# Kernel optimization log

Hardware: AMD Instinct MI355X
Metric: run time of the kernel (lower is better)

## Reference

```python
import jax, jax.numpy as jnp
import numpy as np

N = 100000   # nodes
E = 1600000  # edges (before self loops)
F = 64       # num_features
H = 64       # hidden_channels
C = 10       # num_classes
G = 128      # graphs in batch
NEG_SLOPE = 0.2


def setup_inputs() -> dict:
    key = jax.random.key(0)
    ks = jax.random.split(key, 16)
    x = jax.random.normal(ks[0], (N, F), dtype=jnp.float32)
    edge_index = jax.random.randint(ks[1], (2, E), 0, N, dtype=jnp.int64)
    batch = jnp.sort(jax.random.randint(ks[2], (N,), 0, G, dtype=jnp.int64))
    def glorot(k, shape):
        fan = shape[0] + shape[-1]
        return jax.random.uniform(k, shape, jnp.float32, -1.0, 1.0) * np.sqrt(6.0 / fan)
    return {
        "x": x, "edge_index": edge_index, "batch": batch,
        # GATConv 1 (F -> H)
        "W1": glorot(ks[3], (F, H)), "as1": glorot(ks[4], (H,)), "ad1": glorot(ks[5], (H,)), "b1": jnp.zeros((H,), jnp.float32),
        # GATConv 2 (H -> H)
        "W2": glorot(ks[6], (H, H)), "as2": glorot(ks[7], (H,)), "ad2": glorot(ks[8], (H,)), "b2": jnp.zeros((H,), jnp.float32),
        # MLP head
        "mw1": glorot(ks[9], (H, H)), "mb1": jnp.zeros((H,), jnp.float32),
        "mw2": glorot(ks[10], (H, C)), "mb2": jnp.zeros((C,), jnp.float32),
    }


def gat_conv(x, src, dst, W, a_s, a_d, b):
    # x: [N, Fin] -> h: [N, Fout]
    h = x @ W
    # per-node attention halves, gathered per edge (heads=1)
    al_s = h @ a_s   # [N]
    al_d = h @ a_d   # [N]
    e = jax.nn.leaky_relu(al_s[src] + al_d[dst], NEG_SLOPE)  # [E']
    # segment softmax over incoming edges of each destination node
    m = jax.ops.segment_max(e, dst, num_segments=N)
    ex = jnp.exp(e - m[dst])
    denom = jax.ops.segment_sum(ex, dst, num_segments=N)
    alpha = ex / denom[dst]                                   # [E']
    # weighted scatter-add of source features
    out = jax.ops.segment_sum(alpha[:, None] * h[src], dst, num_segments=N)
    return out + b


def reference(x, edge_index, batch, W1, as1, ad1, b1, W2, as2, ad2, b2, mw1, mb1, mw2, mb2):
    # add self loops (PyG GATConv default)
    loop = jnp.arange(N, dtype=edge_index.dtype)
    src = jnp.concatenate([edge_index[0], loop])
    dst = jnp.concatenate([edge_index[1], loop])

    h = gat_conv(x, src, dst, W1, as1, ad1, b1)
    h = jax.nn.elu(h)  # dropout p=0.5 is identity in eval mode
    h = gat_conv(h, src, dst, W2, as2, ad2, b2)
    h = jax.nn.elu(h)

    h = jax.nn.relu(h @ mw1 + mb1) @ mw2 + mb2   # MLP [N, C]
    return jax.ops.segment_sum(h, batch, num_segments=G)  # global_add_pool [G, C]
```

## Files before the change

kernel.cpp:

```cpp
#include <hip/hip_runtime.h>
#include <hip/hip_bf16.h>
#include <math.h>

#define SHIFT 20.0f
#define T_PER 16
#define TILE (256 * T_PER)
#define SEG_CAP 12288
#define BCAP 10240

typedef __bf16 bf16x8 __attribute__((ext_vector_type(8)));
typedef float  f32x4  __attribute__((ext_vector_type(4)));

__device__ __forceinline__ unsigned f2bf(float f) {
    unsigned u = __float_as_uint(f);
    return (u + 0x7fffu + ((u >> 16) & 1u)) >> 16;
}

__global__ void init_kernel(int* __restrict__ bcur, int K2,
                            float* __restrict__ Pz, int nPz)
{
    int t = threadIdx.x;
    if (t < K2) bcur[t * 16] = t * BCAP;
    for (int i = t; i < nPz; i += 256) Pz[i] = 0.f;
}

__global__ __launch_bounds__(256) void multisplit_kernel(
    const int* __restrict__ esrc, const int* __restrict__ edst,
    int* __restrict__ bcur, unsigned* __restrict__ pairbuf,
    int nE, int nN, int K2, int nTiles)
{
    __shared__ int lhist[256];
    __shared__ int lbase[256];
    int t = threadIdx.x;
    int tot = nE + nN;

    for (int tile = blockIdx.x; tile < nTiles; tile += gridDim.x) {
        int base = tile * TILE;
        if (t < K2) lhist[t] = 0;
        __syncthreads();

        unsigned pk[T_PER];
        int loc[T_PER];
        #pragma unroll
        for (int i = 0; i < T_PER; i++) {
            int e = base + t + i * 256;
            if (e < tot) {
                int s = (e < nE) ? esrc[e] : (e - nE);
                int d = (e < nE) ? edst[e] : (e - nE);
                int b = d >> 9;
                pk[i] = ((unsigned)s << 9) | (unsigned)(d & 511);
                int idx = atomicAdd(&lhist[b], 1);
                loc[i] = (b << 20) | idx;
            } else loc[i] = -1;
        }
        __syncthreads();
        if (t < K2) {
            int c = lhist[t];
            lbase[t] = (c > 0) ? atomicAdd(&bcur[t * 16], c) : 0;
        }
        __syncthreads();
        #pragma unroll
        for (int i = 0; i < T_PER; i++) {
            if (loc[i] >= 0)
                pairbuf[lbase[loc[i] >> 20] + (loc[i] & 0xFFFFF)] = pk[i];
        }
        __syncthreads();
    }
}

__global__ __launch_bounds__(256) void local_scatter_kernel(
    const unsigned* __restrict__ pairbuf, const int* __restrict__ bcur,
    int2* __restrict__ rp2, int* __restrict__ csr_src, int nN, int K2)
{
    __shared__ unsigned seg[SEG_CAP];
    __shared__ int lh[512];
    __shared__ int cur[512];
    __shared__ int psum[256];
    int b = blockIdx.x;
    int t = threadIdx.x;
    int d0 = b * 512;
    int nd = min(512, nN - d0);
    int lo = b * BCAP;
    int hi = bcur[b * 16];
    int len = hi - lo;
    bool inLds = (len <= SEG_CAP);

    lh[t] = 0; lh[t + 256] = 0;
    if (inLds)
        for (int j = t; j < len; j += 256) seg[j] = pairbuf[lo + j];
    __syncthreads();
    if (inLds) {
        for (int j = t; j < len; j += 256) atomicAdd(&lh[seg[j] & 511u], 1);
    } else {
        for (int j = lo + t; j < hi; j += 256)
            atomicAdd(&lh[pairbuf[j] & 511u], 1);
    }
    __syncthreads();

    int v0 = lh[2 * t], v1 = lh[2 * t + 1];
    int ps = v0 + v1;
    psum[t] = ps;
    __syncthreads();
    for (int off = 1; off < 256; off <<= 1) {
        int u = (t >= off) ? psum[t - off] : 0;
        __syncthreads();
        psum[t] += u;
        __syncthreads();
    }
    int e0 = lo + psum[t] - ps;
    int e1 = e0 + v0;
    cur[2 * t] = e0;
    cur[2 * t + 1] = e1;
    if (2 * t < nd)     rp2[d0 + 2 * t]     = make_int2(e0, v0);
    if (2 * t + 1 < nd) rp2[d0 + 2 * t + 1] = make_int2(e1, v1);
    __syncthreads();

    if (inLds) {
        for (int j = t; j < len; j += 256) {
            unsigned w = seg[j];
            int pos = atomicAdd(&cur[w & 511u], 1);
            csr_src[pos] = (int)(w >> 9);
        }
    } else {
        for (int j = lo + t; j < hi; j += 256) {
            unsigned w = pairbuf[j];
            int pos = atomicAdd(&cur[w & 511u], 1);
            csr_src[pos] = (int)(w >> 9);
        }
    }
}

__global__ void prep_kernel(const float* __restrict__ W1,
                            const float* __restrict__ as1, const float* __restrict__ ad1,
                            const float* __restrict__ W2,
                            const float* __restrict__ as2, const float* __restrict__ ad2,
                            const float* __restrict__ mw1,
                            uint4* __restrict__ Wf1, uint4* __restrict__ Wf2,
                            uint4* __restrict__ mwf)
{
    __shared__ float wasad[256];
    int t = threadIdx.x;
    {
        int k = t & 63;
        const float* W  = (t < 128) ? W1 : W2;
        const float* av = (t < 64) ? as1 : (t < 128) ? ad1 : (t < 192) ? as2 : ad2;
        float s = 0.f;
        for (int n = 0; n < 64; n++) s = fmaf(W[k * 64 + n], av[n], s);
        wasad[t] = s;
    }
    __syncthreads();

    for (int idx = t; idx < 1792; idx += 256) {
        const float* W; const float* wv; uint4* dst; int rem;
        if (idx < 640)       { rem = idx;        W = W1;  wv = &wasad[0];   dst = Wf1; }
        else if (idx < 1280) { rem = idx - 640;  W = W2;  wv = &wasad[128]; dst = Wf2; }
        else                 { rem = idx - 1280; W = mw1; wv = nullptr;     dst = mwf; }
        int pair = rem >> 6, l = rem & 63;
        int tt = pair >> 1, s = pair & 1;
        int kb = s * 32 + (l >> 4) * 8;
        unsigned d[4];
        if (tt < 4) {
            int n = tt * 16 + (l & 15);
            #pragma unroll
            for (int j = 0; j < 4; j++)
                d[j] = f2bf(W[(kb + 2 * j) * 64 + n]) |
                       (f2bf(W[(kb + 2 * j + 1) * 64 + n]) << 16);
        } else {
            int n0 = l & 15;
            #pragma unroll
            for (int j = 0; j < 4; j++) {
                float v0 = (n0 == 0) ? wv[kb + 2 * j]     : (n0 == 1) ? wv[64 + kb + 2 * j]     : 0.f;
                float v1 = (n0 == 0) ? wv[kb + 2 * j + 1] : (n0 == 1) ? wv[64 + kb + 2 * j + 1] : 0.f;
                d[j] = f2bf(v0) | (f2bf(v1) << 16);
            }
        }
        dst[pair * 64 + l] = make_uint4(d[0], d[1], d[2], d[3]);
    }
}

__global__ __launch_bounds__(256) void gemm_att_mfma(
    const void* __restrict__ Xv, int x_is_bf16,
    const uint4* __restrict__ Wf,
    __hip_bfloat16* __restrict__ Hout,
    float* __restrict__ als, float* __restrict__ ald, int nN)
{
    __shared__ __align__(16) unsigned char lds[256 * 144];
    int t = threadIdx.x, lane = t & 63, wv = t >> 6;
    int b0 = blockIdx.x * 256;

    uint4 wf[10];
    #pragma unroll
    for (int p = 0; p < 10; p++) wf[p] = Wf[p * 64 + lane];

    if (x_is_bf16) {
        const uint4* X4 = (const uint4*)Xv;
        int limit = nN * 8;
        #pragma unroll
        for (int k = 0; k < 8; k++) {
            int dst = t + k * 256;
            int idx = b0 * 8 + dst;
            if (idx < limit) {
                int r = dst >> 3, c = dst & 7;
                *(uint4*)(lds + r * 144 + c * 16) = X4[idx];
            }
        }
    } else {
        const float4* Xf = (const float4*)Xv;
        int limit = nN * 16;
        #pragma unroll
        for (int k = 0; k < 16; k++) {
            int dst = t + k * 256;
            int idx = b0 * 16 + dst;
            if (idx < limit) {
                float4 v = Xf[idx];
                uint2 r2;
                r2.x = f2bf(v.x) | (f2bf(v.y) << 16);
                r2.y = f2bf(v.z) | (f2bf(v.w) << 16);
                int r = dst >> 4, c = dst & 15;
                *(uint2*)(lds + r * 144 + c * 8) = r2;
            }
        }
    }
    __syncthreads();

    f32x4 acc[4][5] = {};
    int rbase = wv * 64;
    #pragma unroll
    for (int s = 0; s < 2; s++) {
        #pragma unroll
        for (int rf = 0; rf < 4; rf++) {
            const uint4 av = *(const uint4*)(lds + (rbase + rf * 16 + (lane & 15)) * 144
                                                 + s * 64 + (lane >> 4) * 16);
            bf16x8 a = __builtin_bit_cast(bf16x8, av);
            #pragma unroll
            for (int tt = 0; tt < 5; tt++) {
                bf16x8 b = __builtin_bit_cast(bf16x8, wf[tt * 2 + s]);
                acc[rf][tt] = __builtin_amdgcn_mfma_f32_16x16x32_bf16(a, b, acc[rf][tt], 0, 0, 0);
            }
        }
    }

    int q = lane >> 4, c = lane & 15;
    #pragma unroll
    for (int rf = 0; rf < 4; rf++) {
        #pragma unroll
        for (int r = 0; r < 4; r++) {
            int n = b0 + rbase + rf * 16 + q * 4 + r;
            if (n < nN) {
                #pragma unroll
                for (int tt = 0; tt < 4; tt++)
                    Hout[(size_t)n * 64 + tt * 16 + c] = __float2bfloat16(acc[rf][tt][r]);
                if (c == 0)      als[n] = acc[rf][4][r];
                else if (c == 1) ald[n] = acc[rf][4][r];
            }
        }
    }
}

__global__ __launch_bounds__(256) void pull_kernel(
    const int* __restrict__ csr_src, const int2* __restrict__ rp2,
    const unsigned* __restrict__ Hu,
    const float* __restrict__ als, const float* __restrict__ ald,
    const float* __restrict__ bias,
    __hip_bfloat162* __restrict__ out2, int nN)
{
    int lane = threadIdx.x & 63;
    int half = lane >> 5;
    int fl = lane & 31;
    int wid  = (blockIdx.x * blockDim.x + threadIdx.x) >> 6;
    int nw   = (gridDim.x * blockDim.x) >> 6;
    float2 bl2 = ((const float2*)bias)[fl];

    for (int d = wid; d < nN; d += nw) {
        int2 rp = rp2[d];
        int s0 = rp.x, s1 = rp.x + rp.y;
        float aldd = ald[d];
        float aclo = 0.f, achi = 0.f, den = 0.f;

        for (int base = s0; base < s1; base += 64) {
            int j = base + lane;
            bool v = (j < s1);
            int sl = v ? csr_src[j] : 0;
            float ex = 0.f;
            if (v) {
                float sc = als[sl] + aldd;
                sc = (sc > 0.f) ? sc : 0.2f * sc;
                ex = __expf(sc - SHIFT);
            }
            float es = ex;
            #pragma unroll
            for (int off = 32; off > 0; off >>= 1) es += __shfl_xor(es, off);
            den += es;

            int m = min(64, s1 - base);
            int i2 = 0;
            for (; i2 + 3 < m; i2 += 4) {
                int iA = i2 + half, iB = i2 + 2 + half;
                int sA = __shfl(sl, iA), sB = __shfl(sl, iB);
                float eA = __shfl(ex, iA), eB = __shfl(ex, iB);
                unsigned dA = Hu[(size_t)sA * 32 + fl];
                unsigned dB = Hu[(size_t)sB * 32 + fl];
                aclo = fmaf(eA, __uint_as_float(dA << 16), aclo);
                achi = fmaf(eA, __uint_as_float(dA & 0xffff0000u), achi);
                aclo = fmaf(eB, __uint_as_float(dB << 16), aclo);
                achi = fmaf(eB, __uint_as_float(dB & 0xffff0000u), achi);
            }
            for (; i2 < m; i2 += 2) {
                int idx = i2 + half;
                int s = __shfl(sl, idx);
                float e = (idx < m) ? __shfl(ex, idx) : 0.f;
                unsigned dd = Hu[(size_t)s * 32 + fl];
                aclo = fmaf(e, __uint_as_float(dd << 16), aclo);
                achi = fmaf(e, __uint_as_float(dd & 0xffff0000u), achi);
            }
        }
        aclo += __shfl_xor(aclo, 32);
        achi += __shfl_xor(achi, 32);
        float v0 = aclo / den + bl2.x;
        float v1 = achi / den + bl2.y;
        v0 = (v0 > 0.f) ? v0 : expm1f(v0);
        v1 = (v1 > 0.f) ? v1 : expm1f(v1);
        if (half == 0) {
            __hip_bfloat162 pk;
            pk.x = __float2bfloat16(v0);
            pk.y = __float2bfloat16(v1);
            out2[(size_t)d * 32 + fl] = pk;
        }
    }
}

__global__ __launch_bounds__(256) void mlp_pool_mfma(
    const uint4* __restrict__ Hin,
    const uint4* __restrict__ mwf, const float* __restrict__ mb1,
    const int* __restrict__ batch,
    float* __restrict__ P, float* __restrict__ Pcnt, int nN)
{
    __shared__ __align__(16) unsigned char lds[256 * 144];
    int t = threadIdx.x, lane = t & 63, wv = t >> 6;
    int b0 = blockIdx.x * 256;

    uint4 wf[8];
    #pragma unroll
    for (int p = 0; p < 8; p++) wf[p] = mwf[p * 64 + lane];

    int limit = nN * 8;
    #pragma unroll
    for (int k = 0; k < 8; k++) {
        int dst = t + k * 256;
        int idx = b0 * 8 + dst;
        if (idx < limit) {
            int r = dst >> 3, c = dst & 7;
            *(uint4*)(lds + r * 144 + c * 16) = Hin[idx];
        }
    }
    __syncthreads();

    f32x4 acc[4][4] = {};
    int rbase = wv * 64;
    #pragma unroll
    for (int s = 0; s < 2; s++) {
        #pragma unroll
        for (int rf = 0; rf < 4; rf++) {
            const uint4 av = *(const uint4*)(lds + (rbase + rf * 16 + (lane & 15)) * 144
                                                 + s * 64 + (lane >> 4) * 16);
            bf16x8 a = __builtin_bit_cast(bf16x8, av);
            #pragma unroll
            for (int tt = 0; tt < 4; tt++) {
                bf16x8 b = __builtin_bit_cast(bf16x8, wf[tt * 2 + s]);
                acc[rf][tt] = __builtin_amdgcn_mfma_f32_16x16x32_bf16(a, b, acc[rf][tt], 0, 0, 0);
            }
        }
    }

    int q = lane >> 4, c = lane & 15;
    float bl0 = mb1[c], bl1 = mb1[16 + c], bl2 = mb1[32 + c], bl3 = mb1[48 + c];
    float r0 = 0.f, r1 = 0.f, r2 = 0.f, r3 = 0.f, ccnt = 0.f;
    int gcur = -1;
    #pragma unroll
    for (int rf = 0; rf < 4; rf++) {
        #pragma unroll
        for (int r = 0; r < 4; r++) {
            int n = b0 + rbase + rf * 16 + q * 4 + r;
            if (n < nN) {
                int g = batch[n];
                if (g != gcur) {
                    if (gcur >= 0) {
                        atomicAdd(&P[(size_t)gcur * 64 + c],      r0);
                        atomicAdd(&P[(size_t)gcur * 64 + 16 + c], r1);
                        atomicAdd(&P[(size_t)gcur * 64 + 32 + c], r2);
                        atomicAdd(&P[(size_t)gcur * 64 + 48 + c], r3);
                        if (c == 0) atomicAdd(&Pcnt[gcur], ccnt);
                    }
                    gcur = g; r0 = r1 = r2 = r3 = 0.f; ccnt = 0.f;
                }
                r0 += fmaxf(acc[rf][0][r] + bl0, 0.f);
                r1 += fmaxf(acc[rf][1][r] + bl1, 0.f);
                r2 += fmaxf(acc[rf][2][r] + bl2, 0.f);
                r3 += fmaxf(acc[rf][3][r] + bl3, 0.f);
                ccnt += 1.f;
            }
        }
    }
    if (gcur >= 0) {
        atomicAdd(&P[(size_t)gcur * 64 + c],      r0);
        atomicAdd(&P[(size_t)gcur * 64 + 16 + c], r1);
        atomicAdd(&P[(size_t)gcur * 64 + 32 + c], r2);
        atomicAdd(&P[(size_t)gcur * 64 + 48 + c], r3);
        if (c == 0) atomicAdd(&Pcnt[gcur], ccnt);
    }
}

__global__ void head_out_kernel(const float* __restrict__ P,
                                const float* __restrict__ Pcnt,
                                const float* __restrict__ mw2,
                                const float* __restrict__ mb2,
                                float* __restrict__ out, int nOut)
{
    int t = blockIdx.x * blockDim.x + threadIdx.x;
    if (t >= nOut) return;
    int g = t / 10, j = t % 10;
    float s = mb2[j] * Pcnt[g];
    const float* pr = P + (size_t)g * 64;
    #pragma unroll
    for (int k = 0; k < 64; k++) s = fmaf(pr[k], mw2[k * 10 + j], s);
    out[t] = s;
}

extern "C" void kernel_launch(void* const* d_in, const int* in_sizes, int n_in,
                              void* d_out, int out_size, void* d_ws, size_t ws_size,
                              hipStream_t stream)
{
    const float* x   = (const float*)d_in[0];
    const int*  eidx = (const int*)d_in[1];
    const int* batch = (const int*)d_in[2];
    const float* W1  = (const float*)d_in[3];
    const float* as1 = (const float*)d_in[4];
    const float* ad1 = (const float*)d_in[5];
    const float* b1  = (const float*)d_in[6];
    const float* W2  = (const float*)d_in[7];
    const float* as2 = (const float*)d_in[8];
    const float* ad2 = (const float*)d_in[9];
    const float* b2  = (const float*)d_in[10];
    const float* mw1 = (const float*)d_in[11];
    const float* mb1 = (const float*)d_in[12];
    const float* mw2 = (const float*)d_in[13];
    const float* mb2 = (const float*)d_in[14];
    float* out = (float*)d_out;

    int nN = in_sizes[0] / 64;
    int nE = in_sizes[1] / 2;
    int tot = nE + nN;
    int K2 = (nN + 511) >> 9;
    int G  = out_size / 10;
    const int* esrc = eidx;
    const int* edst = eidx + nE;

    float* ws = (float*)d_ws;
    size_t NF = (size_t)nN * 64;
    size_t capTot = (size_t)K2 * BCAP;
    float* bufA   = ws;
    float* bufB   = ws + NF;
    float* als    = ws + 2 * NF;
    float* ald    = als + nN;
    int2* rp2     = (int2*)(ald + nN);
    int* csr_src  = (int*)(rp2 + nN);
    int* bcur     = csr_src + capTot;
    float* P      = (float*)(bcur + K2 * 16 + 15);
    float* Pcnt   = P + (size_t)G * 64;
    uintptr_t wb  = ((uintptr_t)(Pcnt + G) + 255) & ~(uintptr_t)255;
    uint4* Wf1    = (uint4*)wb;
    uint4* Wf2    = Wf1 + 640;
    uint4* mwf    = Wf2 + 640;
    unsigned* pairbuf = (unsigned*)bufA;
    __hip_bfloat16* hbf = (__hip_bfloat16*)bufB;

    dim3 blk(256);
    int nTiles = (tot + TILE - 1) / TILE;
    int nT256 = (nN + 255) / 256;

    init_kernel<<<1, blk, 0, stream>>>(bcur, K2, P, G * 64 + G);
    multisplit_kernel<<<nTiles, blk, 0, stream>>>(esrc, edst, bcur, pairbuf,
                                                  nE, nN, K2, nTiles);
    local_scatter_kernel<<<K2, blk, 0, stream>>>(pairbuf, bcur, rp2,
                                                 csr_src, nN, K2);

    prep_kernel<<<1, blk, 0, stream>>>(W1, as1, ad1, W2, as2, ad2, mw1,
                                       Wf1, Wf2, mwf);

    gemm_att_mfma<<<nT256, blk, 0, stream>>>(x, 0, Wf1, hbf, als, ald, nN);
    pull_kernel<<<2048, blk, 0, stream>>>(csr_src, rp2, (const unsigned*)hbf,
                                          als, ald, b1,
                                          (__hip_bfloat162*)bufA, nN);
    gemm_att_mfma<<<nT256, blk, 0, stream>>>(bufA, 1, Wf2, hbf, als, ald, nN);
    pull_kernel<<<2048, blk, 0, stream>>>(csr_src, rp2, (const unsigned*)hbf,
                                          als, ald, b2,
                                          (__hip_bfloat162*)bufA, nN);

    mlp_pool_mfma<<<nT256, blk, 0, stream>>>((const uint4*)bufA, mwf, mb1,
                                             batch, P, Pcnt, nN);
    head_out_kernel<<<(out_size + 255) / 256, blk, 0, stream>>>(P, Pcnt, mw2,
                                                                mb2, out, out_size);
}
```

Measured before the change: 303.7 us.

## Fuse setup kernels, co-schedule multisplit with first GEMM, widen local scatter

Merges init and weight-prep into one two-block setup kernel. Runs the edge multisplit and the first-layer GEMM as disjoint block ranges of a single launch, since they are independent. Halves the per-block edge tile and raises local_scatter to 1024 threads with a 512-wide scan. The aim is fewer launches and better occupancy in the CSR build stages, at the cost of more blocks doing bcur atomics and heavier register/LDS use in the fused kernel.

```diff
diff --git a/kernel.cpp b/kernel.cpp
--- a/kernel.cpp
+++ b/kernel.cpp
@@ -3,10 +3,11 @@
 #include <math.h>
 
 #define SHIFT 20.0f
-#define T_PER 16
+#define T_PER 8
 #define TILE (256 * T_PER)
 #define SEG_CAP 12288
 #define BCAP 10240
+#define LS_T 1024
 
 typedef __bf16 bf16x8 __attribute__((ext_vector_type(8)));
 typedef float  f32x4  __attribute__((ext_vector_type(4)));
@@ -16,130 +17,23 @@
     return (u + 0x7fffu + ((u >> 16) & 1u)) >> 16;
 }
 
-__global__ void init_kernel(int* __restrict__ bcur, int K2,
-                            float* __restrict__ Pz, int nPz)
+__global__ void setup_kernel(int* __restrict__ bcur, int K2,
+                             float* __restrict__ Pz, int nPz,
+                             const float* __restrict__ W1,
+                             const float* __restrict__ as1, const float* __restrict__ ad1,
+                             const float* __restrict__ W2,
+                             const float* __restrict__ as2, const float* __restrict__ ad2,
+                             const float* __restrict__ mw1,
+                             uint4* __restrict__ Wf1, uint4* __restrict__ Wf2,
+                             uint4* __restrict__ mwf)
 {
     int t = threadIdx.x;
-    if (t < K2) bcur[t * 16] = t * BCAP;
-    for (int i = t; i < nPz; i += 256) Pz[i] = 0.f;
-}
-
-__global__ __launch_bounds__(256) void multisplit_kernel(
-    const int* __restrict__ esrc, const int* __restrict__ edst,
-    int* __restrict__ bcur, unsigned* __restrict__ pairbuf,
-    int nE, int nN, int K2, int nTiles)
-{
-    __shared__ int lhist[256];
-    __shared__ int lbase[256];
-    int t = threadIdx.x;
-    int tot = nE + nN;
-
-    for (int tile = blockIdx.x; tile < nTiles; tile += gridDim.x) {
-        int base = tile * TILE;
-        if (t < K2) lhist[t] = 0;
-        __syncthreads();
-
-        unsigned pk[T_PER];
-        int loc[T_PER];
-        #pragma unroll
-        for (int i = 0; i < T_PER; i++) {
-            int e = base + t + i * 256;
-            if (e < tot) {
-                int s = (e < nE) ? esrc[e] : (e - nE);
-                int d = (e < nE) ? edst[e] : (e - nE);
-                int b = d >> 9;
-                pk[i] = ((unsigned)s << 9) | (unsigned)(d & 511);
-                int idx = atomicAdd(&lhist[b], 1);
-                loc[i] = (b << 20) | idx;
-            } else loc[i] = -1;
-        }
-        __syncthreads();
-        if (t < K2) {
-            int c = lhist[t];
-            lbase[t] = (c > 0) ? atomicAdd(&bcur[t * 16], c) : 0;
-        }
-        __syncthreads();
-        #pragma unroll
-        for (int i = 0; i < T_PER; i++) {
-            if (loc[i] >= 0)
-                pairbuf[lbase[loc[i] >> 20] + (loc[i] & 0xFFFFF)] = pk[i];
-        }
-        __syncthreads();
-    }
-}
-
-__global__ __launch_bounds__(256) void local_scatter_kernel(
-    const unsigned* __restrict__ pairbuf, const int* __restrict__ bcur,
-    int2* __restrict__ rp2, int* __restrict__ csr_src, int nN, int K2)
-{
-    __shared__ unsigned seg[SEG_CAP];
-    __shared__ int lh[512];
-    __shared__ int cur[512];
-    __shared__ int psum[256];
-    int b = blockIdx.x;
-    int t = threadIdx.x;
-    int d0 = b * 512;
-    int nd = min(512, nN - d0);
-    int lo = b * BCAP;
-    int hi = bcur[b * 16];
-    int len = hi - lo;
-    bool inLds = (len <= SEG_CAP);
-
-    lh[t] = 0; lh[t + 256] = 0;
-    if (inLds)
-        for (int j = t; j < len; j += 256) seg[j] = pairbuf[lo + j];
-    __syncthreads();
-    if (inLds) {
-        for (int j = t; j < len; j += 256) atomicAdd(&lh[seg[j] & 511u], 1);
-    } else {
-        for (int j = lo + t; j < hi; j += 256)
-            atomicAdd(&lh[pairbuf[j] & 511u], 1);
-    }
-    __syncthreads();
-
-    int v0 = lh[2 * t], v1 = lh[2 * t + 1];
-    int ps = v0 + v1;
-    psum[t] = ps;
-    __syncthreads();
-    for (int off = 1; off < 256; off <<= 1) {
-        int u = (t >= off) ? psum[t - off] : 0;
-        __syncthreads();
-        psum[t] += u;
-        __syncthreads();
-    }
-    int e0 = lo + psum[t] - ps;
-    int e1 = e0 + v0;
-    cur[2 * t] = e0;
-    cur[2 * t + 1] = e1;
-    if (2 * t < nd)     rp2[d0 + 2 * t]     = make_int2(e0, v0);
-    if (2 * t + 1 < nd) rp2[d0 + 2 * t + 1] = make_int2(e1, v1);
-    __syncthreads();
-
-    if (inLds) {
-        for (int j = t; j < len; j += 256) {
-            unsigned w = seg[j];
-            int pos = atomicAdd(&cur[w & 511u], 1);
-            csr_src[pos] = (int)(w >> 9);
-        }
-    } else {
-        for (int j = lo + t; j < hi; j += 256) {
-            unsigned w = pairbuf[j];
-            int pos = atomicAdd(&cur[w & 511u], 1);
-            csr_src[pos] = (int)(w >> 9);
-        }
-    }
-}
-
-__global__ void prep_kernel(const float* __restrict__ W1,
-                            const float* __restrict__ as1, const float* __restrict__ ad1,
-                            const float* __restrict__ W2,
-                            const float* __restrict__ as2, const float* __restrict__ ad2,
-                            const float* __restrict__ mw1,
-                            uint4* __restrict__ Wf1, uint4* __restrict__ Wf2,
-                            uint4* __restrict__ mwf)
-{
+    if (blockIdx.x == 0) {
+        if (t < K2) bcur[t * 16] = t * BCAP;
+        for (int i = t; i < nPz; i += 256) Pz[i] = 0.f;
+        return;
+    }
     __shared__ float wasad[256];
-    int t = threadIdx.x;
     {
         int k = t & 63;
         const float* W  = (t < 128) ? W1 : W2;
@@ -178,15 +72,51 @@
     }
 }
 
-__global__ __launch_bounds__(256) void gemm_att_mfma(
-    const void* __restrict__ Xv, int x_is_bf16,
-    const uint4* __restrict__ Wf,
-    __hip_bfloat16* __restrict__ Hout,
-    float* __restrict__ als, float* __restrict__ ald, int nN)
-{
-    __shared__ __align__(16) unsigned char lds[256 * 144];
+__device__ __forceinline__ void multisplit_body(
+    unsigned char* lds, const int* __restrict__ esrc, const int* __restrict__ edst,
+    int* __restrict__ bcur, unsigned* __restrict__ pairbuf,
+    int nE, int tot, int K2, int tile)
+{
+    int* lhist = (int*)lds;
+    int* lbase = lhist + 256;
+    int t = threadIdx.x;
+    int base = tile * TILE;
+    if (t < K2) lhist[t] = 0;
+    __syncthreads();
+
+    unsigned pk[T_PER];
+    int loc[T_PER];
+    #pragma unroll
+    for (int i = 0; i < T_PER; i++) {
+        int e = base + t + i * 256;
+        if (e < tot) {
+            int s = (e < nE) ? esrc[e] : (e - nE);
+            int d = (e < nE) ? edst[e] : (e - nE);
+            int b = d >> 9;
+            pk[i] = ((unsigned)s << 9) | (unsigned)(d & 511);
+            int idx = atomicAdd(&lhist[b], 1);
+            loc[i] = (b << 20) | idx;
+        } else loc[i] = -1;
+    }
+    __syncthreads();
+    if (t < K2) {
+        int c = lhist[t];
+        lbase[t] = (c > 0) ? atomicAdd(&bcur[t * 16], c) : 0;
+    }
+    __syncthreads();
+    #pragma unroll
+    for (int i = 0; i < T_PER; i++) {
+        if (loc[i] >= 0)
+            pairbuf[lbase[loc[i] >> 20] + (loc[i] & 0xFFFFF)] = pk[i];
+    }
+}
+
+__device__ __forceinline__ void gemm_body(
+    unsigned char* lds, const void* __restrict__ Xv, int x_is_bf16,
+    const uint4* __restrict__ Wf, __hip_bfloat16* __restrict__ Hout,
+    float* __restrict__ als, float* __restrict__ ald, int nN, int b0)
+{
     int t = threadIdx.x, lane = t & 63, wv = t >> 6;
-    int b0 = blockIdx.x * 256;
 
     uint4 wf[10];
     #pragma unroll
@@ -253,6 +183,92 @@
                 if (c == 0)      als[n] = acc[rf][4][r];
                 else if (c == 1) ald[n] = acc[rf][4][r];
             }
+        }
+    }
+}
+
+__global__ __launch_bounds__(256) void ms_gemm_kernel(
+    const int* __restrict__ esrc, const int* __restrict__ edst,
+    int* __restrict__ bcur, unsigned* __restrict__ pairbuf,
+    int nE, int nN, int K2, int nTiles,
+    const void* __restrict__ Xv, const uint4* __restrict__ Wf,
+    __hip_bfloat16* __restrict__ Hout,
+    float* __restrict__ als, float* __restrict__ ald)
+{
+    __shared__ __align__(16) unsigned char lds[256 * 144];
+    if (blockIdx.x < nTiles) {
+        multisplit_body(lds, esrc, edst, bcur, pairbuf, nE, nE + nN, K2, blockIdx.x);
+    } else {
+        gemm_body(lds, Xv, 0, Wf, Hout, als, ald, nN, (blockIdx.x - nTiles) * 256);
+    }
+}
+
+__global__ __launch_bounds__(256) void gemm_att_mfma(
+    const void* __restrict__ Xv, int x_is_bf16,
+    const uint4* __restrict__ Wf,
+    __hip_bfloat16* __restrict__ Hout,
+    float* __restrict__ als, float* __restrict__ ald, int nN)
+{
+    __shared__ __align__(16) unsigned char lds[256 * 144];
+    gemm_body(lds, Xv, x_is_bf16, Wf, Hout, als, ald, nN, blockIdx.x * 256);
+}
+
+__global__ __launch_bounds__(LS_T) void local_scatter_kernel(
+    const unsigned* __restrict__ pairbuf, const int* __restrict__ bcur,
+    int2* __restrict__ rp2, int* __restrict__ csr_src, int nN, int K2)
+{
+    __shared__ unsigned seg[SEG_CAP];
+    __shared__ int lh[512];
+    __shared__ int cur[512];
+    __shared__ int psum[512];
+    int b = blockIdx.x;
+    int t = threadIdx.x;
+    int d0 = b * 512;
+    int nd = min(512, nN - d0);
+    int lo = b * BCAP;
+    int hi = bcur[b * 16];
+    int len = hi - lo;
+    bool inLds = (len <= SEG_CAP);
+
+    if (t < 512) lh[t] = 0;
+    if (inLds)
+        for (int j = t; j < len; j += LS_T) seg[j] = pairbuf[lo + j];
+    __syncthreads();
+    if (inLds) {
+        for (int j = t; j < len; j += LS_T) atomicAdd(&lh[seg[j] & 511u], 1);
+    } else {
+        for (int j = lo + t; j < hi; j += LS_T)
+            atomicAdd(&lh[pairbuf[j] & 511u], 1);
+    }
+    __syncthreads();
+
+    int v = (t < 512) ? lh[t] : 0;
+    if (t < 512) psum[t] = v;
+    __syncthreads();
+    for (int off = 1; off < 512; off <<= 1) {
+        int u = (t < 512 && t >= off) ? psum[t - off] : 0;
+        __syncthreads();
+        if (t < 512) psum[t] += u;
+        __syncthreads();
+    }
+    if (t < 512) {
+        int e0 = lo + psum[t] - v;
+        cur[t] = e0;
+        if (t < nd) rp2[d0 + t] = make_int2(e0, v);
+    }
+    __syncthreads();
+
+    if (inLds) {
+        for (int j = t; j < len; j += LS_T) {
+            unsigned w = seg[j];
+            int pos = atomicAdd(&cur[w & 511u], 1);
+            csr_src[pos] = (int)(w >> 9);
+        }
+    } else {
+        for (int j = lo + t; j < hi; j += LS_T) {
+            unsigned w = pairbuf[j];
+            int pos = atomicAdd(&cur[w & 511u], 1);
+            csr_src[pos] = (int)(w >> 9);
         }
     }
 }
@@ -478,16 +494,15 @@
     int nTiles = (tot + TILE - 1) / TILE;
     int nT256 = (nN + 255) / 256;
 
-    init_kernel<<<1, blk, 0, stream>>>(bcur, K2, P, G * 64 + G);
-    multisplit_kernel<<<nTiles, blk, 0, stream>>>(esrc, edst, bcur, pairbuf,
-                                                  nE, nN, K2, nTiles);
-    local_scatter_kernel<<<K2, blk, 0, stream>>>(pairbuf, bcur, rp2,
-                                                 csr_src, nN, K2);
-
-    prep_kernel<<<1, blk, 0, stream>>>(W1, as1, ad1, W2, as2, ad2, mw1,
-                                       Wf1, Wf2, mwf);
-
-    gemm_att_mfma<<<nT256, blk, 0, stream>>>(x, 0, Wf1, hbf, als, ald, nN);
+    setup_kernel<<<2, blk, 0, stream>>>(bcur, K2, P, G * 64 + G,
+                                        W1, as1, ad1, W2, as2, ad2, mw1,
+                                        Wf1, Wf2, mwf);
+    ms_gemm_kernel<<<nTiles + nT256, blk, 0, stream>>>(
+        esrc, edst, bcur, pairbuf, nE, nN, K2, nTiles,
+        x, Wf1, hbf, als, ald);
+    local_scatter_kernel<<<K2, dim3(LS_T), 0, stream>>>(pairbuf, bcur, rp2,
+                                                        csr_src, nN, K2);
+
     pull_kernel<<<2048, blk, 0, stream>>>(csr_src, rp2, (const unsigned*)hbf,
                                           als, ald, b1,
                                           (__hip_bfloat162*)bufA, nN);
```

After: 302.5 us. About the same (-0.4%).
